# Optimization experiments

Measured on AMD Instinct MI355X. Metric: run time of the kernel, lower is better.

Reference implementation:

```python
import jax, jax.numpy as jnp
import numpy as np


def _layernorm(x, g, b, eps=1e-6):
    mu = jnp.mean(x, -1, keepdims=True)
    var = jnp.var(x, -1, keepdims=True)
    return (x - mu) * jax.lax.rsqrt(var + eps) * g + b


def _rope_interleave(x, cos, sin):
    # de-interleave pairs (x0,x1),(x2,x3),... -> [evens | odds]  (matches
    # torch view(..., d//2, 2).transpose(-1,-2).reshape(..., d))
    x = jnp.concatenate([x[..., 0::2], x[..., 1::2]], axis=-1)
    d = x.shape[-1]
    x1, x2 = x[..., : d // 2], x[..., d // 2 :]
    rot = jnp.concatenate([-x2, x1], axis=-1)
    return x * cos + rot * sin


def setup_inputs() -> dict:
    key = jax.random.key(0)
    k = jax.random.split(key, 6)
    T, H, D, R, HID, QLR, K = 2048, 32, 128, 64, 4096, 1536, 256
    hidden_states = jax.random.normal(k[0], (1, T, HID), jnp.float32)
    q_latent = jax.random.normal(k[1], (1, T, QLR), jnp.float32)
    wq_b = jax.random.normal(k[2], (QLR, H * D), jnp.float32) * 0.02
    wk = jax.random.normal(k[3], (HID, D), jnp.float32) * 0.02
    w_proj = jax.random.normal(k[4], (HID, H), jnp.float32) * 0.02
    k_gamma = jnp.ones((D,), jnp.float32)
    k_beta = jnp.zeros((D,), jnp.float32)
    # real rotary cos/sin tables for the 64-dim rope slice
    pos = jnp.arange(T, dtype=jnp.float32)
    inv_freq = 1.0 / (10000.0 ** (jnp.arange(0, R, 2, dtype=jnp.float32) / R))
    freqs = jnp.outer(pos, inv_freq)
    emb = jnp.concatenate([freqs, freqs], axis=-1)  # [T, R]
    cos, sin = jnp.cos(emb), jnp.sin(emb)
    ks = jnp.zeros((T,), jnp.int32)
    ke = jnp.arange(1, T + 1, dtype=jnp.int32)  # causal: keys [0, t]
    return dict(hidden_states=hidden_states, q_latent=q_latent, ks=ks, ke=ke,
                cos=cos, sin=sin, wq_b=wq_b, wk=wk, k_gamma=k_gamma,
                k_beta=k_beta, w_proj=w_proj, index_topk=K)


def reference(hidden_states, q_latent, ks, ke, cos, sin, wq_b, wk,
              k_gamma, k_beta, w_proj, index_topk):
    T = hidden_states.shape[1]
    H = w_proj.shape[1]
    D = wk.shape[1]
    R = cos.shape[-1]
    weight_scale = (D ** -0.5) * (H ** -0.5)

    q = (q_latent[0] @ wq_b).reshape(T, H, D)              # [T,H,D]
    k = _layernorm(hidden_states[0] @ wk, k_gamma, k_beta)  # [T,D]
    w = hidden_states[0] @ w_proj                           # [T,H]

    q_pe = _rope_interleave(q[..., :R], cos[:, None, :], sin[:, None, :])
    k_pe = _rope_interleave(k[..., :R], cos, sin)
    q = jnp.concatenate([q_pe, q[..., R:]], axis=-1)
    k = jnp.concatenate([k_pe, k[..., R:]], axis=-1)

    # lightning-indexer score: I[t,s] = sum_h w[t,h] * relu(q[t,h] . k[s])
    scores = jnp.einsum('thd,sd->ths', q, k)                # [T,H,S]
    scores = jnp.einsum('ths,th->ts', jax.nn.relu(scores), w) * weight_scale

    j = jnp.arange(T)
    mask = (j[None, :] >= ks[:, None]) & (j[None, :] < ke[:, None])
    scores = jnp.where(mask, scores, -1e30)
    values, idx = jax.lax.top_k(scores, index_topk)
    return idx.reshape(1, T, 1, index_topk), values
```

## Files before the change

kernel.cpp:

```cpp
#include <hip/hip_runtime.h>
#include <cstdint>

typedef unsigned short u16;
typedef unsigned int   u32;
typedef unsigned long long u64;

typedef short bf16x8 __attribute__((ext_vector_type(8)));
typedef float f32x4  __attribute__((ext_vector_type(4)));
typedef u16   u16x8  __attribute__((ext_vector_type(8)));

__device__ __forceinline__ u16 f2b(float f){
  u32 u = __float_as_uint(f);
  u += 0x7FFFu + ((u >> 16) & 1u);
  return (u16)(u >> 16);
}
__device__ __forceinline__ float b2f(u16 h){ return __uint_as_float(((u32)h) << 16); }
__device__ __forceinline__ u32 fkey(float f){
  u32 u = __float_as_uint(f);
  return u ^ ((u & 0x80000000u) ? 0xFFFFFFFFu : 0x80000000u);
}
__device__ __forceinline__ float unkey(u32 k){
  u32 u = (k & 0x80000000u) ? (k ^ 0x80000000u) : ~k;
  return __uint_as_float(u);
}
__device__ __forceinline__ void gload16(const void* g, void* l){
  __builtin_amdgcn_global_load_lds(
      reinterpret_cast<const __attribute__((address_space(1))) char*>(reinterpret_cast<uintptr_t>(g)),
      reinterpret_cast<__attribute__((address_space(3))) char*>(reinterpret_cast<uintptr_t>(l)),
      16, 0, 0);
}

__global__ __launch_bounds__(256) void k_cvt(const float* __restrict__ in, u16* __restrict__ out, int n8){
  int i = blockIdx.x * 256 + threadIdx.x;
  if (i >= n8) return;
  const float4* p = (const float4*)in + (size_t)i * 2;
  float4 a = p[0], b = p[1];
  u16x8 v;
  v[0]=f2b(a.x); v[1]=f2b(a.y); v[2]=f2b(a.z); v[3]=f2b(a.w);
  v[4]=f2b(b.x); v[5]=f2b(b.y); v[6]=f2b(b.z); v[7]=f2b(b.w);
  *((u16x8*)out + i) = v;
}

__global__ __launch_bounds__(256) void k_tcvt(const float* __restrict__ in, u16* __restrict__ out, int R, int C){
  __shared__ float tile[32][33];
  int c0 = blockIdx.x * 32, r0 = blockIdx.y * 32;
  int tx = threadIdx.x & 31, ty = threadIdx.x >> 5;
  for (int i = 0; i < 4; i++){
    int r = ty * 4 + i;
    tile[r][tx] = in[(size_t)(r0 + r) * C + c0 + tx];
  }
  __syncthreads();
  for (int i = 0; i < 4; i++){
    int c = ty * 4 + i;
    out[(size_t)(c0 + c) * R + r0 + tx] = f2b(tile[tx][c]);
  }
}

__global__ __launch_bounds__(256) void k_wct(const float* __restrict__ wk, const float* __restrict__ wp, u16* __restrict__ out){
  __shared__ float tile[32][33];
  int c0 = blockIdx.x * 32, i0 = blockIdx.y * 32;
  int tx = threadIdx.x & 31, ty = threadIdx.x >> 5;
  for (int j = 0; j < 4; j++){
    int i = i0 + ty * 4 + j;
    int c = c0 + tx;
    float v = 0.f;
    if (c < 128) v = wk[(size_t)i * 128 + c];
    else if (c < 160) v = wp[(size_t)i * 32 + (c - 128)];
    tile[ty * 4 + j][tx] = v;
  }
  __syncthreads();
  for (int j = 0; j < 4; j++){
    int c = c0 + ty * 4 + j;
    out[(size_t)c * 4096 + i0 + tx] = f2b(tile[tx][ty * 4 + j]);
  }
}

__global__ __launch_bounds__(256) void k_gemm_kw(const float* __restrict__ A, const u16* __restrict__ B, float* __restrict__ Cp){
  const int Kd = 4096, NC = 192;
  __shared__ float As[128 * 64];
  __shared__ u16 Bs[64 * 64];
  int lin = blockIdx.x;
  int xcd = lin & 7, idx = lin >> 3;
  int nb = idx % 3, pz = idx / 3;
  int p = xcd + 8 * pz;
  int m0 = (p & 15) * 128;
  int kt0 = (p >> 4) * 512;
  int n0 = nb * 64;
  float* C = Cp + (size_t)(p >> 4) * 2048 * NC;
  int tid = threadIdx.x, lane = tid & 63, wid = tid >> 6;
  int wm = wid * 32;
  f32x4 acc[2][4] = {};
  for (int kt = kt0; kt < kt0 + 512; kt += 64){
    for (int c = tid; c < 2048; c += 256){
      int row = c >> 4, off = (c & 15) * 4;
      gload16(A + (size_t)(m0 + row) * Kd + kt + off, (float*)As + (size_t)c * 4);
    }
    for (int c = tid; c < 512; c += 256){
      int row = c >> 3, off = (c & 7) * 8;
      gload16(B + (size_t)(n0 + row) * Kd + kt + off, (u16*)Bs + (size_t)c * 8);
    }
    __syncthreads();
    for (int kk = 0; kk < 2; kk++){
      bf16x8 af[2], bfr[4];
      for (int i = 0; i < 2; i++){
        const float* src = &As[(wm + i * 16 + (lane & 15)) * 64 + kk * 32 + (lane >> 4) * 8];
        f32x4 lo = *(const f32x4*)&src[0];
        f32x4 hi = *(const f32x4*)&src[4];
        bf16x8 t;
        t[0]=(short)f2b(lo[0]); t[1]=(short)f2b(lo[1]); t[2]=(short)f2b(lo[2]); t[3]=(short)f2b(lo[3]);
        t[4]=(short)f2b(hi[0]); t[5]=(short)f2b(hi[1]); t[6]=(short)f2b(hi[2]); t[7]=(short)f2b(hi[3]);
        af[i] = t;
      }
      for (int j = 0; j < 4; j++)
        bfr[j] = *(const bf16x8*)&Bs[(j * 16 + (lane & 15)) * 64 + kk * 32 + (lane >> 4) * 8];
      for (int i = 0; i < 2; i++)
        for (int j = 0; j < 4; j++)
          acc[i][j] = __builtin_amdgcn_mfma_f32_16x16x32_bf16(af[i], bfr[j], acc[i][j], 0, 0, 0);
    }
    __syncthreads();
  }
  for (int i = 0; i < 2; i++)
    for (int j = 0; j < 4; j++){
      int row = m0 + wm + i * 16 + ((lane >> 4) * 4);
      int col = n0 + j * 16 + (lane & 15);
      for (int r = 0; r < 4; r++)
        C[(size_t)(row + r) * NC + col] = acc[i][j][r];
    }
}

__global__ __launch_bounds__(256) void k_lnrope(const float* __restrict__ kwp, const float* __restrict__ gamma,
                                                const float* __restrict__ beta, const float* __restrict__ cosp,
                                                const float* __restrict__ sinp, u16* __restrict__ krot,
                                                float* __restrict__ wfin){
  const size_t ZS = (size_t)2048 * 192;
  int row = blockIdx.x * 4 + (threadIdx.x >> 6);
  int lane = threadIdx.x & 63;
  const float* x = kwp + (size_t)row * 192;
  float2 v = {0.f, 0.f};
  for (int z = 0; z < 8; z++){
    float2 p = *(const float2*)&x[z * ZS + lane * 2];
    v.x += p.x; v.y += p.y;
  }
  float s = v.x + v.y, ss = v.x * v.x + v.y * v.y;
  for (int o = 32; o; o >>= 1){ s += __shfl_xor(s, o); ss += __shfl_xor(ss, o); }
  float mu = s * (1.f / 128.f);
  float var = ss * (1.f / 128.f) - mu * mu;
  float rs = rsqrtf(var + 1e-6f);
  float y0 = (v.x - mu) * rs * gamma[lane * 2]     + beta[lane * 2];
  float y1 = (v.y - mu) * rs * gamma[lane * 2 + 1] + beta[lane * 2 + 1];
  u16* out = krot + (size_t)row * 128;
  if (lane < 32){
    float c = cosp[(size_t)row * 64 + lane], sn = sinp[(size_t)row * 64 + lane];
    out[lane]      = f2b(y0 * c - y1 * sn);
    out[lane + 32] = f2b(y1 * c + y0 * sn);
    float wsum = 0.f;
    for (int z = 0; z < 8; z++) wsum += x[z * ZS + 128 + lane];
    wfin[(size_t)row * 32 + lane] = wsum;
  } else {
    out[lane * 2]     = f2b(y0);
    out[lane * 2 + 1] = f2b(y1);
  }
}

__global__ __launch_bounds__(256) void k_gemm_q(const u16* __restrict__ A, const u16* __restrict__ B, u16* __restrict__ C){
  const int N = 4096, Kd = 1536;
  __shared__ u16 As[128 * 64];
  __shared__ u16 Bs[128 * 64];
  int linb = blockIdx.x;
  int xcd = linb & 7, loc = linb >> 3;
  int n0 = (xcd * 4 + (loc >> 4)) * 128;
  int m0 = (loc & 15) * 128;
  int tid = threadIdx.x, lane = tid & 63, wid = tid >> 6;
  int wm = (wid >> 1) * 64, wn = (wid & 1) * 64;
  f32x4 acc[4][4] = {};
  for (int kt = 0; kt < Kd; kt += 64){
    for (int c = tid; c < 1024; c += 256){
      int row = c >> 3, off = (c & 7) * 8;
      gload16(A + (size_t)(m0 + row) * Kd + kt + off, (u16*)As + (size_t)c * 8);
      gload16(B + (size_t)(n0 + row) * Kd + kt + off, (u16*)Bs + (size_t)c * 8);
    }
    __syncthreads();
    for (int kk = 0; kk < 2; kk++){
      bf16x8 af[4], bfr[4];
      for (int i = 0; i < 4; i++){
        af[i]  = *(const bf16x8*)&As[(wm + i * 16 + (lane & 15)) * 64 + kk * 32 + (lane >> 4) * 8];
        bfr[i] = *(const bf16x8*)&Bs[(wn + i * 16 + (lane & 15)) * 64 + kk * 32 + (lane >> 4) * 8];
      }
      for (int i = 0; i < 4; i++)
        for (int j = 0; j < 4; j++)
          acc[i][j] = __builtin_amdgcn_mfma_f32_16x16x32_bf16(af[i], bfr[j], acc[i][j], 0, 0, 0);
    }
    __syncthreads();
  }
  for (int i = 0; i < 4; i++)
    for (int j = 0; j < 4; j++){
      int row = m0 + wm + i * 16 + ((lane >> 4) * 4);
      int col = n0 + wn + j * 16 + (lane & 15);
      for (int r = 0; r < 4; r++)
        C[(size_t)(row + r) * N + col] = f2b(acc[i][j][r]);
    }
}

__global__ __launch_bounds__(256) void k_ropeq(u16* __restrict__ q, const float* __restrict__ cosp, const float* __restrict__ sinp){
  int seg = blockIdx.x * 4 + (threadIdx.x >> 6);
  int lane = threadIdx.x & 63;
  int t = seg >> 5, h = seg & 31;
  u16* p = q + (size_t)t * 4096 + h * 128;
  float x = b2f(p[lane]);
  float ve = __shfl(x, (lane & 31) * 2);
  float vo = __shfl(x, (lane & 31) * 2 + 1);
  float c = cosp[(size_t)t * 64 + lane], s = sinp[(size_t)t * 64 + lane];
  float r = (lane < 32) ? (ve * c - vo * s) : (vo * c + ve * s);
  p[lane] = f2b(r);
}

__global__ __launch_bounds__(256, 4) void k_scores(const u16* __restrict__ q, const u16* __restrict__ krot,
                                                   const float* __restrict__ wfin, const int* __restrict__ ks,
                                                   const int* __restrict__ ke, float* __restrict__ S){
  __shared__ u16 Bs[128 * 128];
  __shared__ float Ws[32][32];
  __shared__ int keL[32], ksL[32];
  int bid = blockIdx.x;
  int xcd = bid & 7, loc = bid >> 3;
  int sb = loc & 15, j0 = loc >> 4;
  int tb = j0 * 8 + xcd;
  int t0 = tb * 32, s0 = sb * 128;
  int tid = threadIdx.x, lane = tid & 63, wid = tid >> 6;
  int wr = wid >> 1, wc = wid & 1;

  int kev = ke[t0 + (lane & 31)];
  int kemax = kev;
  for (int o = 16; o; o >>= 1) kemax = max(kemax, __shfl_xor(kemax, o));
  if (s0 >= kemax) return;

  for (int c = tid; c < 2048; c += 256)
    gload16(krot + (size_t)(s0 + (c >> 4)) * 128 + (c & 15) * 8, (u16*)Bs + (size_t)c * 8);
  for (int i = tid; i < 1024; i += 256){
    int h = i >> 5, r = i & 31;
    Ws[h][r] = wfin[(size_t)(t0 + r) * 32 + h];
  }
  if (tid < 32){ keL[tid] = ke[t0 + tid]; ksL[tid] = ks[t0 + tid]; }
  __syncthreads();

  bf16x8 bfr[4][4];
  for (int j = 0; j < 4; j++)
    for (int kc = 0; kc < 4; kc++)
      bfr[j][kc] = *(const bf16x8*)&Bs[(wc * 64 + j * 16 + (lane & 15)) * 128 + kc * 32 + (lane >> 4) * 8];

  f32x4 acc[4] = {};
  const u16* qbase = q + ((size_t)t0 + wr * 16 + (lane & 15)) * 4096 + (lane >> 4) * 8;
  int rbase = wr * 16 + ((lane >> 4) * 4);
  for (int h = 0; h < 32; h++){
    bf16x8 af[4];
    for (int kc = 0; kc < 4; kc++)
      af[kc] = *(const bf16x8*)&qbase[h * 128 + kc * 32];
    f32x4 ah[4] = {};
    for (int kc = 0; kc < 4; kc++)
      for (int j = 0; j < 4; j++)
        ah[j] = __builtin_amdgcn_mfma_f32_16x16x32_bf16(af[kc], bfr[j][kc], ah[j], 0, 0, 0);
    for (int r = 0; r < 4; r++){
      float wv = Ws[h][rbase + r];
      for (int j = 0; j < 4; j++)
        acc[j][r] += fmaxf(ah[j][r], 0.f) * wv;
    }
  }
  const float scale = 0.015625f;
  for (int j = 0; j < 4; j++){
    int col = s0 + wc * 64 + j * 16 + (lane & 15);
    for (int r = 0; r < 4; r++){
      int row = rbase + r;
      bool valid = (col >= ksL[row]) && (col < keL[row]);
      S[(size_t)(t0 + row) * 2048 + col] = valid ? acc[j][r] * scale : -1e30f;
    }
  }
}

__global__ __launch_bounds__(256) void k_topk(const float* __restrict__ S, const int* __restrict__ ktp,
                                              const int* __restrict__ ke, float* __restrict__ out){
  int t = blockIdx.x;
  int T = gridDim.x;
  const float* row = S + (size_t)t * 2048;
  __shared__ u32 keys[2048];
  __shared__ u32 hist[256];
  __shared__ u32 ssum[256];
  __shared__ u32 sb, srem;
  __shared__ u32 wtot[8];
  __shared__ int selIdx[256];
  __shared__ u32 baseGt, baseTie;
  __shared__ u64 skey[256];
  int tid = threadIdx.x;
  int K = ktp[0]; if (K > 256) K = 256;
  int ket = ke[t]; if (ket < 0) ket = 0; if (ket > 2048) ket = 2048;
  int limit = (ket + 255) & ~255;
  if (limit < 256) limit = 256;
  if (limit > 2048) limit = 2048;
  const u32 kneg = fkey(-1e30f);
  for (int i4 = tid; i4 < (limit >> 2); i4 += 256){
    int base = i4 * 4;
    if (base + 4 <= ket){
      float4 v = ((const float4*)row)[i4];
      keys[base + 0] = fkey(v.x); keys[base + 1] = fkey(v.y);
      keys[base + 2] = fkey(v.z); keys[base + 3] = fkey(v.w);
    } else {
      for (int e = 0; e < 4; e++){
        int i = base + e;
        keys[i] = (i < ket) ? fkey(row[i]) : kneg;
      }
    }
  }
  __syncthreads();
  if (limit > K){
    u32 prefix = 0, pmask = 0, rem = (u32)K;
    for (int p = 3; p >= 0; p--){
      int sh = p * 8;
      hist[tid] = 0;
      __syncthreads();
      for (int i = tid; i < limit; i += 256){
        u32 u = keys[i];
        if ((u & pmask) == prefix) atomicAdd(&hist[(u >> sh) & 255], 1u);
      }
      __syncthreads();
      ssum[tid] = hist[tid];
      __syncthreads();
      for (int off = 1; off < 256; off <<= 1){
        u32 add = (tid + off < 256) ? ssum[tid + off] : 0u;
        __syncthreads();
        ssum[tid] += add;
        __syncthreads();
      }
      u32 mine = ssum[tid];
      u32 above = (tid == 255) ? 0u : ssum[tid + 1];
      if (mine >= rem && above < rem){ sb = (u32)tid; srem = rem - above; }
      __syncthreads();
      prefix |= (sb << sh);
      pmask |= (255u << sh);
      rem = srem;
      __syncthreads();
    }
    u32 thr = prefix;
    int G = K - (int)rem;
    if (tid == 0){ baseGt = 0; baseTie = 0; }
    __syncthreads();
    int nch = limit >> 8;
    for (int ch = 0; ch < nch; ch++){
      int i = ch * 256 + tid;
      u32 u = keys[i];
      bool gt = (u > thr), tie = (u == thr);
      u64 bg = __ballot(gt), bt = __ballot(tie);
      int lane = tid & 63, w = tid >> 6;
      if (lane == 0){ wtot[w] = (u32)__popcll(bg); wtot[4 + w] = (u32)__popcll(bt); }
      __syncthreads();
      u32 og = baseGt, ot = baseTie;
      for (int ww = 0; ww < w; ww++){ og += wtot[ww]; ot += wtot[4 + ww]; }
      og += (u32)__popcll(bg & ((1ull << lane) - 1ull));
      ot += (u32)__popcll(bt & ((1ull << lane) - 1ull));
      if (gt) selIdx[og] = i;
      else if (tie && ot < rem) selIdx[G + ot] = i;
      __syncthreads();
      if (tid == 0){
        for (int ww = 0; ww < 4; ww++){ baseGt += wtot[ww]; baseTie += wtot[4 + ww]; }
      }
      __syncthreads();
    }
    if (tid < K){
      int si = selIdx[tid];
      u32 u = keys[si];
      skey[tid] = ((u64)(~u) << 32) | (u32)si;
    } else {
      skey[tid] = ~0ull;
    }
  } else {
    if (tid < K) skey[tid] = ((u64)(~keys[tid]) << 32) | (u32)tid;
    else skey[tid] = ~0ull;
  }
  __syncthreads();
  for (int size = 2; size <= 256; size <<= 1){
    for (int stride = size >> 1; stride > 0; stride >>= 1){
      int p = tid ^ stride;
      if (p > tid){
        bool up = ((tid & size) == 0);
        u64 a = skey[tid], b = skey[p];
        if ((a > b) == up){ skey[tid] = b; skey[p] = a; }
      }
      __syncthreads();
    }
  }
  if (tid < K){
    u64 sk = skey[tid];
    int idx = (int)(u32)(sk & 0xFFFFFFFFu);
    float val = unkey(~(u32)(sk >> 32));
    out[(size_t)t * K + tid] = (float)idx;
    out[(size_t)T * K + (size_t)t * K + tid] = val;
  }
}

extern "C" void kernel_launch(void* const* d_in, const int* in_sizes, int n_in,
                              void* d_out, int out_size, void* d_ws, size_t ws_size,
                              hipStream_t stream){
  const float* hs   = (const float*)d_in[0];
  const float* ql   = (const float*)d_in[1];
  const int*   ks   = (const int*)  d_in[2];
  const int*   ke   = (const int*)  d_in[3];
  const float* cosp = (const float*)d_in[4];
  const float* sinp = (const float*)d_in[5];
  const float* wqb  = (const float*)d_in[6];
  const float* wk   = (const float*)d_in[7];
  const float* kg   = (const float*)d_in[8];
  const float* kb   = (const float*)d_in[9];
  const float* wp   = (const float*)d_in[10];
  const int*   ktp  = (const int*)  d_in[11];

  char* w = (char*)d_ws;
  u16* qlb = (u16*)w;  w += (size_t)2048 * 1536 * 2;
  u16* wqT = (u16*)w;  w += (size_t)4096 * 1536 * 2;
  u16* wct = (u16*)w;  w += (size_t)192 * 4096 * 2;
  u16* qb  = (u16*)w;  w += (size_t)2048 * 4096 * 2;
  float* kwp = (float*)w; w += (size_t)8 * 2048 * 192 * 4;
  float* wfin = (float*)w; w += (size_t)2048 * 32 * 4;
  u16* krt = (u16*)w;  w += (size_t)2048 * 128 * 2;
  float* S  = (float*)w; w += (size_t)2048 * 2048 * 4;

  hipLaunchKernelGGL(k_cvt, dim3(1536), dim3(256), 0, stream, ql, qlb, 393216);
  hipLaunchKernelGGL(k_tcvt, dim3(128, 48), dim3(256), 0, stream, wqb, wqT, 1536, 4096);
  hipLaunchKernelGGL(k_wct, dim3(6, 128), dim3(256), 0, stream, wk, wp, wct);
  hipLaunchKernelGGL(k_gemm_kw, dim3(384), dim3(256), 0, stream, hs, wct, kwp);
  hipLaunchKernelGGL(k_lnrope, dim3(512), dim3(256), 0, stream, kwp, kg, kb, cosp, sinp, krt, wfin);
  hipLaunchKernelGGL(k_gemm_q, dim3(512), dim3(256), 0, stream, qlb, wqT, qb);
  hipLaunchKernelGGL(k_ropeq, dim3(16384), dim3(256), 0, stream, qb, cosp, sinp);
  hipLaunchKernelGGL(k_scores, dim3(1024), dim3(256), 0, stream, qb, krt, wfin, ks, ke, S);
  hipLaunchKernelGGL(k_topk, dim3(2048), dim3(256), 0, stream, S, ktp, ke, (float*)d_out);
}
```

Baseline: 184.0 us.

## Fuse q rope into GEMM epilogue and split score heads across two blocks

```diff
diff --git a/kernel.cpp b/kernel.cpp
--- a/kernel.cpp
+++ b/kernel.cpp
@@ -162,7 +162,9 @@
   }
 }
 
-__global__ __launch_bounds__(256) void k_gemm_q(const u16* __restrict__ A, const u16* __restrict__ B, u16* __restrict__ C){
+__global__ __launch_bounds__(256) void k_gemm_q(const u16* __restrict__ A, const u16* __restrict__ B,
+                                                const float* __restrict__ cosp, const float* __restrict__ sinp,
+                                                u16* __restrict__ C){
   const int N = 4096, Kd = 1536;
   __shared__ u16 As[128 * 64];
   __shared__ u16 Bs[128 * 64];
@@ -192,6 +194,32 @@
     }
     __syncthreads();
   }
+  if (wn == 0){
+    int l = lane & 15;
+    int base = lane & 48;
+    int sl = base + ((2 * l) & 15);
+    for (int i = 0; i < 4; i++){
+      int rowb = m0 + wm + i * 16 + ((lane >> 4) * 4);
+      f32x4 ne[4];
+      for (int j = 0; j < 4; j++){
+        int jj = j & 1;
+        for (int r = 0; r < 4; r++){
+          float eA = __shfl(acc[i][2 * jj][r],     sl);
+          float eB = __shfl(acc[i][2 * jj + 1][r], sl);
+          float oA = __shfl(acc[i][2 * jj][r],     sl + 1);
+          float oB = __shfl(acc[i][2 * jj + 1][r], sl + 1);
+          float e = (l >= 8) ? eB : eA;
+          float o = (l >= 8) ? oB : oA;
+          int row = rowb + r;
+          int d = j * 16 + l;
+          float c = cosp[(size_t)row * 64 + d];
+          float s = sinp[(size_t)row * 64 + d];
+          ne[j][r] = (j < 2) ? (e * c - o * s) : (o * c + e * s);
+        }
+      }
+      for (int j = 0; j < 4; j++) acc[i][j] = ne[j];
+    }
+  }
   for (int i = 0; i < 4; i++)
     for (int j = 0; j < 4; j++){
       int row = m0 + wm + i * 16 + ((lane >> 4) * 4);
@@ -201,28 +229,15 @@
     }
 }
 
-__global__ __launch_bounds__(256) void k_ropeq(u16* __restrict__ q, const float* __restrict__ cosp, const float* __restrict__ sinp){
-  int seg = blockIdx.x * 4 + (threadIdx.x >> 6);
-  int lane = threadIdx.x & 63;
-  int t = seg >> 5, h = seg & 31;
-  u16* p = q + (size_t)t * 4096 + h * 128;
-  float x = b2f(p[lane]);
-  float ve = __shfl(x, (lane & 31) * 2);
-  float vo = __shfl(x, (lane & 31) * 2 + 1);
-  float c = cosp[(size_t)t * 64 + lane], s = sinp[(size_t)t * 64 + lane];
-  float r = (lane < 32) ? (ve * c - vo * s) : (vo * c + ve * s);
-  p[lane] = f2b(r);
-}
-
 __global__ __launch_bounds__(256, 4) void k_scores(const u16* __restrict__ q, const u16* __restrict__ krot,
-                                                   const float* __restrict__ wfin, const int* __restrict__ ks,
-                                                   const int* __restrict__ ke, float* __restrict__ S){
+                                                   const float* __restrict__ wfin, const int* __restrict__ ke,
+                                                   float* __restrict__ S0, float* __restrict__ S1){
   __shared__ u16 Bs[128 * 128];
-  __shared__ float Ws[32][32];
-  __shared__ int keL[32], ksL[32];
+  __shared__ float Ws[16][32];
   int bid = blockIdx.x;
   int xcd = bid & 7, loc = bid >> 3;
-  int sb = loc & 15, j0 = loc >> 4;
+  int hgrp = loc & 1, rest = loc >> 1;
+  int sb = rest & 15, j0 = rest >> 4;
   int tb = j0 * 8 + xcd;
   int t0 = tb * 32, s0 = sb * 128;
   int tid = threadIdx.x, lane = tid & 63, wid = tid >> 6;
@@ -235,11 +250,10 @@
 
   for (int c = tid; c < 2048; c += 256)
     gload16(krot + (size_t)(s0 + (c >> 4)) * 128 + (c & 15) * 8, (u16*)Bs + (size_t)c * 8);
-  for (int i = tid; i < 1024; i += 256){
+  for (int i = tid; i < 512; i += 256){
     int h = i >> 5, r = i & 31;
-    Ws[h][r] = wfin[(size_t)(t0 + r) * 32 + h];
-  }
-  if (tid < 32){ keL[tid] = ke[t0 + tid]; ksL[tid] = ks[t0 + tid]; }
+    Ws[h][r] = wfin[(size_t)(t0 + r) * 32 + hgrp * 16 + h];
+  }
   __syncthreads();
 
   bf16x8 bfr[4][4];
@@ -248,9 +262,9 @@
       bfr[j][kc] = *(const bf16x8*)&Bs[(wc * 64 + j * 16 + (lane & 15)) * 128 + kc * 32 + (lane >> 4) * 8];
 
   f32x4 acc[4] = {};
-  const u16* qbase = q + ((size_t)t0 + wr * 16 + (lane & 15)) * 4096 + (lane >> 4) * 8;
+  const u16* qbase = q + ((size_t)t0 + wr * 16 + (lane & 15)) * 4096 + (size_t)hgrp * 16 * 128 + (lane >> 4) * 8;
   int rbase = wr * 16 + ((lane >> 4) * 4);
-  for (int h = 0; h < 32; h++){
+  for (int h = 0; h < 16; h++){
     bf16x8 af[4];
     for (int kc = 0; kc < 4; kc++)
       af[kc] = *(const bf16x8*)&qbase[h * 128 + kc * 32];
@@ -264,22 +278,21 @@
         acc[j][r] += fmaxf(ah[j][r], 0.f) * wv;
     }
   }
-  const float scale = 0.015625f;
+  float* Sp = hgrp ? S1 : S0;
   for (int j = 0; j < 4; j++){
     int col = s0 + wc * 64 + j * 16 + (lane & 15);
-    for (int r = 0; r < 4; r++){
-      int row = rbase + r;
-      bool valid = (col >= ksL[row]) && (col < keL[row]);
-      S[(size_t)(t0 + row) * 2048 + col] = valid ? acc[j][r] * scale : -1e30f;
-    }
-  }
-}
-
-__global__ __launch_bounds__(256) void k_topk(const float* __restrict__ S, const int* __restrict__ ktp,
+    for (int r = 0; r < 4; r++)
+      Sp[(size_t)(t0 + rbase + r) * 2048 + col] = acc[j][r];
+  }
+}
+
+__global__ __launch_bounds__(256) void k_topk(const float* __restrict__ S0, const float* __restrict__ S1,
+                                              const int* __restrict__ ktp, const int* __restrict__ ksv,
                                               const int* __restrict__ ke, float* __restrict__ out){
   int t = blockIdx.x;
   int T = gridDim.x;
-  const float* row = S + (size_t)t * 2048;
+  const float* r0 = S0 + (size_t)t * 2048;
+  const float* r1 = S1 + (size_t)t * 2048;
   __shared__ u32 keys[2048];
   __shared__ u32 hist[256];
   __shared__ u32 ssum[256];
@@ -291,22 +304,22 @@
   int tid = threadIdx.x;
   int K = ktp[0]; if (K > 256) K = 256;
   int ket = ke[t]; if (ket < 0) ket = 0; if (ket > 2048) ket = 2048;
+  int kst = ksv[t]; if (kst < 0) kst = 0;
   int limit = (ket + 255) & ~255;
   if (limit < 256) limit = 256;
   if (limit > 2048) limit = 2048;
   const u32 kneg = fkey(-1e30f);
+  const float scale = 0.015625f;
   for (int i4 = tid; i4 < (limit >> 2); i4 += 256){
     int base = i4 * 4;
-    if (base + 4 <= ket){
-      float4 v = ((const float4*)row)[i4];
-      keys[base + 0] = fkey(v.x); keys[base + 1] = fkey(v.y);
-      keys[base + 2] = fkey(v.z); keys[base + 3] = fkey(v.w);
-    } else {
-      for (int e = 0; e < 4; e++){
-        int i = base + e;
-        keys[i] = (i < ket) ? fkey(row[i]) : kneg;
-      }
-    }
+    float4 a = ((const float4*)r0)[i4];
+    float4 b = ((const float4*)r1)[i4];
+    float v0 = (a.x + b.x) * scale, v1 = (a.y + b.y) * scale;
+    float v2 = (a.z + b.z) * scale, v3 = (a.w + b.w) * scale;
+    keys[base + 0] = (base + 0 >= kst && base + 0 < ket) ? fkey(v0) : kneg;
+    keys[base + 1] = (base + 1 >= kst && base + 1 < ket) ? fkey(v1) : kneg;
+    keys[base + 2] = (base + 2 >= kst && base + 2 < ket) ? fkey(v2) : kneg;
+    keys[base + 3] = (base + 3 >= kst && base + 3 < ket) ? fkey(v3) : kneg;
   }
   __syncthreads();
   if (limit > K){
@@ -418,15 +431,15 @@
   float* kwp = (float*)w; w += (size_t)8 * 2048 * 192 * 4;
   float* wfin = (float*)w; w += (size_t)2048 * 32 * 4;
   u16* krt = (u16*)w;  w += (size_t)2048 * 128 * 2;
-  float* S  = (float*)w; w += (size_t)2048 * 2048 * 4;
+  float* S0 = (float*)w; w += (size_t)2048 * 2048 * 4;
+  float* S1 = (float*)d_ws;
 
   hipLaunchKernelGGL(k_cvt, dim3(1536), dim3(256), 0, stream, ql, qlb, 393216);
   hipLaunchKernelGGL(k_tcvt, dim3(128, 48), dim3(256), 0, stream, wqb, wqT, 1536, 4096);
   hipLaunchKernelGGL(k_wct, dim3(6, 128), dim3(256), 0, stream, wk, wp, wct);
   hipLaunchKernelGGL(k_gemm_kw, dim3(384), dim3(256), 0, stream, hs, wct, kwp);
   hipLaunchKernelGGL(k_lnrope, dim3(512), dim3(256), 0, stream, kwp, kg, kb, cosp, sinp, krt, wfin);
-  hipLaunchKernelGGL(k_gemm_q, dim3(512), dim3(256), 0, stream, qlb, wqT, qb);
-  hipLaunchKernelGGL(k_ropeq, dim3(16384), dim3(256), 0, stream, qb, cosp, sinp);
-  hipLaunchKernelGGL(k_scores, dim3(1024), dim3(256), 0, stream, qb, krt, wfin, ks, ke, S);
-  hipLaunchKernelGGL(k_topk, dim3(2048), dim3(256), 0, stream, S, ktp, ke, (float*)d_out);
-}
+  hipLaunchKernelGGL(k_gemm_q, dim3(512), dim3(256), 0, stream, qlb, wqT, cosp, sinp, qb);
+  hipLaunchKernelGGL(k_scores, dim3(2048), dim3(256), 0, stream, qb, krt, wfin, ke, S0, S1);
+  hipLaunchKernelGGL(k_topk, dim3(2048), dim3(256), 0, stream, S0, S1, ktp, ks, ke, (float*)d_out);
+}
```

Result: faster. 163.0 us (-11.4%).
